# Optimization experiments

Measured on AMD Instinct MI355X. Metric: run time of the kernel, lower is better.

The kernel has to match this reference:

```python
import jax, jax.numpy as jnp
import numpy as np

TEMPERATURE = 0.1

def setup_inputs() -> dict:
    key = jax.random.key(0)
    k1, k2 = jax.random.split(key)
    A = jax.random.normal(k1, (16, 2048, 256), dtype=jnp.float32)
    B = jax.random.normal(k2, (16, 2048, 256), dtype=jnp.float32)
    return {"A": A, "B": B}

def _l2norm(x):
    # F.normalize(p=2, dim=-1): x / max(||x||, eps), eps=1e-12
    n = jnp.sqrt(jnp.sum(x * x, axis=-1, keepdims=True))
    return x / jnp.maximum(n, 1e-12)

def _nce_dir(sim):
    # sim: (B, N, N) logits; labels are the diagonal (row n -> col n)
    # mean over all B*N rows of (logsumexp(row) - row[label])
    lse = jax.nn.logsumexp(sim, axis=-1)            # (B, N)
    diag = jnp.diagonal(sim, axis1=-2, axis2=-1)    # (B, N)
    return jnp.mean(lse - diag)

def reference(A, B):
    emb1 = _l2norm(A)
    emb2 = _l2norm(B)
    sim12 = jnp.einsum("bnc,bmc->bnm", emb1, emb2) / TEMPERATURE  # (B, N, N)
    # sim21 is sim12 transposed per batch; reuse instead of a second bmm
    sim21 = jnp.swapaxes(sim12, -1, -2)
    return _nce_dir(sim12) + _nce_dir(sim21)
```

## Files before the change

### kernel.cpp

```cpp
#include <hip/hip_runtime.h>
#include <hip/hip_bf16.h>

typedef __attribute__((ext_vector_type(8))) __bf16 bf16x8;
typedef __attribute__((ext_vector_type(16))) float f32x16;

#define SCALE_L2E 14.4269504088896f
#define NTOT 32768

#define AS_GLOBAL __attribute__((address_space(1)))
#define AS_LDS    __attribute__((address_space(3)))

__device__ inline void async_copy16(const void* g, void* l) {
    __builtin_amdgcn_global_load_lds((const AS_GLOBAL void*)g, (AS_LDS void*)l, 16, 0, 0);
}

__device__ inline unsigned int f2bf(float f) {
    unsigned int u = __builtin_bit_cast(unsigned int, f);
    u += 0x7fffu + ((u >> 16) & 1u);
    return u >> 16;
}

__device__ inline uint4 pack8(float4 x, float4 y, float s) {
    uint4 r;
    r.x = f2bf(x.x * s) | (f2bf(x.y * s) << 16);
    r.y = f2bf(x.z * s) | (f2bf(x.w * s) << 16);
    r.z = f2bf(y.x * s) | (f2bf(y.y * s) << 16);
    r.w = f2bf(y.z * s) | (f2bf(y.w * s) << 16);
    return r;
}

__device__ inline float sum8(float4 x, float4 y) {
    return x.x + x.y + x.z + x.w + y.x + y.y + y.z + y.w;
}
__device__ inline float dot8(float4 x, float4 y) {
    return x.x*y.x + x.y*y.y + x.z*y.z + x.w*y.w;
}

__global__ __launch_bounds__(256) void nrm_kernel(
        const float* __restrict__ A, const float* __restrict__ B,
        uint4* __restrict__ E1f, uint4* __restrict__ E2f,
        float* __restrict__ diagPart) {
    const int tid = threadIdx.x, w = tid >> 6, l = tid & 63;
    const int q = l & 31, h = l >> 5;
    const int wid = blockIdx.x * 4 + w;

    const float4* A4 = (const float4*)A + ((size_t)wid * 8 + h) * 64 + q * 2;
    const float4* B4 = (const float4*)B + ((size_t)wid * 8 + h) * 64 + q * 2;

    float ddAcc = 0.f;
    float4 a0 = A4[0], a1 = A4[1], b0 = B4[0], b1 = B4[1];

    #pragma unroll
    for (int i = 0; i < 4; ++i) {
        float4 na0, na1, nb0, nb1;
        if (i < 3) {
            const float4* An = A4 + (i + 1) * 128;
            const float4* Bn = B4 + (i + 1) * 128;
            na0 = An[0]; na1 = An[1]; nb0 = Bn[0]; nb1 = Bn[1];
        }
        float sa = dot8(a0, a0) + dot8(a1, a1);
        float sb = dot8(b0, b0) + dot8(b1, b1);
        float dd = dot8(a0, b0) + dot8(a1, b1);
        #pragma unroll
        for (int off = 1; off <= 16; off <<= 1) {
            sa += __shfl_xor(sa, off);
            sb += __shfl_xor(sb, off);
            dd += __shfl_xor(dd, off);
        }
        const float ia = 1.0f / fmaxf(sqrtf(sa), 1e-12f);
        const float ib = 1.0f / fmaxf(sqrtf(sb), 1e-12f);
        if (q == 0) ddAcc += dd * ia * ib * 10.0f;

        const int n0 = wid * 8 + i * 2 + h;
        const size_t chunk = (size_t)(n0 >> 11) * 65536
                           + (size_t)((n0 & 2047) >> 5) * 1024
                           + (q >> 1) * 64 + (q & 1) * 32 + (n0 & 31);
        E1f[chunk] = pack8(a0, a1, ia);
        E2f[chunk] = pack8(b0, b1, ib);

        a0 = na0; a1 = na1; b0 = nb0; b1 = nb1;
    }

    #pragma unroll
    for (int off = 1; off <= 32; off <<= 1) ddAcc += __shfl_xor(ddAcc, off);
    __shared__ float part[4];
    if (l == 0) part[w] = ddAcc;
    __syncthreads();
    if (tid == 0) diagPart[blockIdx.x] = part[0] + part[1] + part[2] + part[3];
}

__global__ __launch_bounds__(256, 2) void gemm_kernel(
        const bf16x8* __restrict__ E1f, const uint4* __restrict__ E2f,
        float* __restrict__ colSum, float* __restrict__ rowSum) {
    __shared__ bf16x8 Bbuf[2][1024];
    __shared__ float colLDS[2048];

    const int tid = threadIdx.x, w = tid >> 6, l = tid & 63;
    const int rt = blockIdx.x, ct = blockIdx.y, b = blockIdx.z;

    for (int i = l; i < 512; i += 64) colLDS[w * 512 + i] = 0.f;

    const bf16x8* Af0 = E1f + (size_t)b * 65536 + (size_t)(rt * 8 + w * 2) * 1024 + l;
    const bf16x8* Af1 = Af0 + 1024;
    bf16x8 af0[16], af1[16];
    #pragma unroll
    for (int kt = 0; kt < 16; ++kt) { af0[kt] = Af0[kt * 64]; af1[kt] = Af1[kt * 64]; }

    float rowAcc0[16], rowAcc1[16];
    #pragma unroll
    for (int r = 0; r < 16; ++r) { rowAcc0[r] = 0.f; rowAcc1[r] = 0.f; }

    const uint4* Bb = E2f + (size_t)b * 65536 + (size_t)ct * 16384 + l;

    auto stage = [&](int buf, int cg) {
        const uint4* src = Bb + (size_t)cg * 1024 + (w * 4) * 64;
        #pragma unroll
        for (int j = 0; j < 4; ++j)
            async_copy16(src + j * 64, &Bbuf[buf][(w * 4 + j) * 64]);
    };

    stage(0, 0);
    __syncthreads();

    for (int cg = 0; cg < 16; ++cg) {
        if (cg < 15) stage((cg + 1) & 1, cg + 1);

        const bf16x8* Bf = Bbuf[cg & 1];
        f32x16 acc0, acc1;
        #pragma unroll
        for (int r = 0; r < 16; ++r) { acc0[r] = 0.f; acc1[r] = 0.f; }

        #pragma unroll
        for (int kt = 0; kt < 16; ++kt) {
            bf16x8 bfrag = Bf[kt * 64 + l];
            acc0 = __builtin_amdgcn_mfma_f32_32x32x16_bf16(af0[kt], bfrag, acc0, 0, 0, 0);
            acc1 = __builtin_amdgcn_mfma_f32_32x32x16_bf16(af1[kt], bfrag, acc1, 0, 0, 0);
        }

        float p = 0.f;
        #pragma unroll
        for (int r = 0; r < 16; ++r) {
            float e0 = exp2f(fmaf(acc0[r], SCALE_L2E, -SCALE_L2E));
            float e1 = exp2f(fmaf(acc1[r], SCALE_L2E, -SCALE_L2E));
            rowAcc0[r] += e0;
            rowAcc1[r] += e1;
            p += e0 + e1;
        }
        p += __shfl_xor(p, 32);
        if (l < 32) colLDS[w * 512 + cg * 32 + l] += p;
        __syncthreads();
    }

    #pragma unroll
    for (int r = 0; r < 16; ++r) {
        #pragma unroll
        for (int off = 1; off <= 16; off <<= 1) {
            rowAcc0[r] += __shfl_xor(rowAcc0[r], off);
            rowAcc1[r] += __shfl_xor(rowAcc1[r], off);
        }
    }
    if ((l & 31) == 0) {
        float* rs = rowSum + (size_t)b * 2048 + rt * 256 + w * 64 + 4 * (l >> 5);
        #pragma unroll
        for (int r = 0; r < 16; ++r) {
            const int rl = (r & 3) + 8 * (r >> 2);
            atomicAdd(&rs[rl], rowAcc0[r]);
            atomicAdd(&rs[rl + 32], rowAcc1[r]);
        }
    }

    float* gcol = colSum + (size_t)b * 2048 + ct * 512;
    for (int i = tid; i < 512; i += 256) {
        float s = colLDS[i] + colLDS[512 + i] + colLDS[1024 + i] + colLDS[1536 + i];
        atomicAdd(&gcol[i], s);
    }
}

__global__ __launch_bounds__(256) void fin1_kernel(
        const float* __restrict__ red, float* __restrict__ scalars) {
    const int tid = threadIdx.x;
    float s = 0.f;
    #pragma unroll
    for (int k = 0; k < 4; ++k)
        s += logf(red[blockIdx.x * 1024 + k * 256 + tid]);
    #pragma unroll
    for (int off = 1; off <= 32; off <<= 1) s += __shfl_xor(s, off);
    __shared__ float part[4];
    if ((tid & 63) == 0) part[tid >> 6] = s;
    __syncthreads();
    if (tid == 0)
        atomicAdd(&scalars[0], part[0] + part[1] + part[2] + part[3]);
}

__global__ __launch_bounds__(256) void fin2_kernel(
        const float* __restrict__ diagPart, const float* __restrict__ scalars,
        float* __restrict__ out) {
    const int tid = threadIdx.x;
    float d = 0.f;
    for (int i = tid; i < 1024; i += 256) d += diagPart[i];
    #pragma unroll
    for (int off = 1; off <= 32; off <<= 1) d += __shfl_xor(d, off);
    __shared__ float part[4];
    if ((tid & 63) == 0) part[tid >> 6] = d;
    __syncthreads();
    if (tid == 0) {
        const float diag = part[0] + part[1] + part[2] + part[3];
        out[0] = (scalars[0] - 2.0f * diag) / (float)NTOT + 20.0f;
    }
}

extern "C" void kernel_launch(void* const* d_in, const int* in_sizes, int n_in,
                              void* d_out, int out_size, void* d_ws, size_t ws_size,
                              hipStream_t stream) {
    const float* A = (const float*)d_in[0];
    const float* B = (const float*)d_in[1];

    char* w = (char*)d_ws;
    uint4* E1f = (uint4*)w;
    uint4* E2f = (uint4*)(w + (size_t)16 * 1024 * 1024);
    float* colSum = (float*)(w + (size_t)32 * 1024 * 1024);
    float* rowSum = colSum + NTOT;
    float* scalars = rowSum + NTOT;
    float* diagPart = scalars + 2;

    hipMemsetAsync(colSum, 0, (size_t)(2 * NTOT + 2) * 4, stream);

    hipLaunchKernelGGL(nrm_kernel, dim3(1024), dim3(256), 0, stream,
                       A, B, E1f, E2f, diagPart);
    hipLaunchKernelGGL(gemm_kernel, dim3(8, 4, 16), dim3(256), 0, stream,
                       (const bf16x8*)E1f, (const uint4*)E2f, colSum, rowSum);
    hipLaunchKernelGGL(fin1_kernel, dim3(64), dim3(256), 0, stream,
                       colSum, scalars);
    hipLaunchKernelGGL(fin2_kernel, dim3(1), dim3(256), 0, stream,
                       diagPart, scalars, (float*)d_out);
}
```

Baseline: 160.4 us.

## Triple-buffer GEMM staging, drop memset and atomics, fuse finalize kernels

The memset is removed. Global atomics on row and column sums are replaced by per-tile partial buffers that a single fused finalize kernel reduces, and the last block, found through a counter, finishes the diagonal term. The GEMM moves to a 3-deep async LDS ring with explicit vmcnt waits and one barrier per step. The nrm kernel issues all loads up front and folds the exp scale into E1, which removes an FMA per element. The grid is flattened so the batch index varies fastest. This cuts launches and atomic contention, at the cost of extra partial-buffer traffic and more LDS.

Result: slower. 291.2 us (+81.5%).

```diff
diff --git a/kernel.cpp b/kernel.cpp
--- a/kernel.cpp
+++ b/kernel.cpp
@@ -29,9 +29,6 @@
     return r;
 }
 
-__device__ inline float sum8(float4 x, float4 y) {
-    return x.x + x.y + x.z + x.w + y.x + y.y + y.z + y.w;
-}
 __device__ inline float dot8(float4 x, float4 y) {
     return x.x*y.x + x.y*y.y + x.z*y.z + x.w*y.w;
 }
@@ -39,7 +36,8 @@
 __global__ __launch_bounds__(256) void nrm_kernel(
         const float* __restrict__ A, const float* __restrict__ B,
         uint4* __restrict__ E1f, uint4* __restrict__ E2f,
-        float* __restrict__ diagPart) {
+        float* __restrict__ diagPart, float* __restrict__ scalars,
+        unsigned int* __restrict__ counter) {
     const int tid = threadIdx.x, w = tid >> 6, l = tid & 63;
     const int q = l & 31, h = l >> 5;
     const int wid = blockIdx.x * 4 + w;
@@ -47,20 +45,21 @@
     const float4* A4 = (const float4*)A + ((size_t)wid * 8 + h) * 64 + q * 2;
     const float4* B4 = (const float4*)B + ((size_t)wid * 8 + h) * 64 + q * 2;
 
+    float4 a[8], bb[8];
+    #pragma unroll
+    for (int i = 0; i < 4; ++i) {
+        a[2*i]    = A4[i * 128];
+        a[2*i+1]  = A4[i * 128 + 1];
+        bb[2*i]   = B4[i * 128];
+        bb[2*i+1] = B4[i * 128 + 1];
+    }
+
     float ddAcc = 0.f;
-    float4 a0 = A4[0], a1 = A4[1], b0 = B4[0], b1 = B4[1];
-
     #pragma unroll
     for (int i = 0; i < 4; ++i) {
-        float4 na0, na1, nb0, nb1;
-        if (i < 3) {
-            const float4* An = A4 + (i + 1) * 128;
-            const float4* Bn = B4 + (i + 1) * 128;
-            na0 = An[0]; na1 = An[1]; nb0 = Bn[0]; nb1 = Bn[1];
-        }
-        float sa = dot8(a0, a0) + dot8(a1, a1);
-        float sb = dot8(b0, b0) + dot8(b1, b1);
-        float dd = dot8(a0, b0) + dot8(a1, b1);
+        float sa = dot8(a[2*i], a[2*i]) + dot8(a[2*i+1], a[2*i+1]);
+        float sb = dot8(bb[2*i], bb[2*i]) + dot8(bb[2*i+1], bb[2*i+1]);
+        float dd = dot8(a[2*i], bb[2*i]) + dot8(a[2*i+1], bb[2*i+1]);
         #pragma unroll
         for (int off = 1; off <= 16; off <<= 1) {
             sa += __shfl_xor(sa, off);
@@ -75,10 +74,8 @@
         const size_t chunk = (size_t)(n0 >> 11) * 65536
                            + (size_t)((n0 & 2047) >> 5) * 1024
                            + (q >> 1) * 64 + (q & 1) * 32 + (n0 & 31);
-        E1f[chunk] = pack8(a0, a1, ia);
-        E2f[chunk] = pack8(b0, b1, ib);
-
-        a0 = na0; a1 = na1; b0 = nb0; b1 = nb1;
+        E1f[chunk] = pack8(a[2*i], a[2*i+1], ia * SCALE_L2E);
+        E2f[chunk] = pack8(bb[2*i], bb[2*i+1], ib);
     }
 
     #pragma unroll
@@ -87,16 +84,18 @@
     if (l == 0) part[w] = ddAcc;
     __syncthreads();
     if (tid == 0) diagPart[blockIdx.x] = part[0] + part[1] + part[2] + part[3];
+    if (blockIdx.x == 0 && tid == 0) { scalars[0] = 0.f; *counter = 0u; }
 }
 
 __global__ __launch_bounds__(256, 2) void gemm_kernel(
         const bf16x8* __restrict__ E1f, const uint4* __restrict__ E2f,
-        float* __restrict__ colSum, float* __restrict__ rowSum) {
-    __shared__ bf16x8 Bbuf[2][1024];
+        float* __restrict__ colPart, float* __restrict__ rowPart) {
+    __shared__ bf16x8 Bbuf[3][1024];
     __shared__ float colLDS[2048];
 
     const int tid = threadIdx.x, w = tid >> 6, l = tid & 63;
-    const int rt = blockIdx.x, ct = blockIdx.y, b = blockIdx.z;
+    const int rt = blockIdx.x >> 6;
+    const int ct = (blockIdx.x >> 4) & 3, b = blockIdx.x & 15;
 
     for (int i = l; i < 512; i += 64) colLDS[w * 512 + i] = 0.f;
 
@@ -120,12 +119,16 @@
     };
 
     stage(0, 0);
-    __syncthreads();
-
+    stage(1, 1);
+
+    #pragma unroll
     for (int cg = 0; cg < 16; ++cg) {
-        if (cg < 15) stage((cg + 1) & 1, cg + 1);
-
-        const bf16x8* Bf = Bbuf[cg & 1];
+        if (cg < 15) asm volatile("s_waitcnt vmcnt(4)" ::: "memory");
+        else         asm volatile("s_waitcnt vmcnt(0)" ::: "memory");
+        __builtin_amdgcn_s_barrier();
+        if (cg < 14) stage((cg + 2) % 3, cg + 2);
+
+        const bf16x8* Bf = Bbuf[cg % 3];
         f32x16 acc0, acc1;
         #pragma unroll
         for (int r = 0; r < 16; ++r) { acc0[r] = 0.f; acc1[r] = 0.f; }
@@ -140,15 +143,14 @@
         float p = 0.f;
         #pragma unroll
         for (int r = 0; r < 16; ++r) {
-            float e0 = exp2f(fmaf(acc0[r], SCALE_L2E, -SCALE_L2E));
-            float e1 = exp2f(fmaf(acc1[r], SCALE_L2E, -SCALE_L2E));
+            float e0 = exp2f(acc0[r] - SCALE_L2E);
+            float e1 = exp2f(acc1[r] - SCALE_L2E);
             rowAcc0[r] += e0;
             rowAcc1[r] += e1;
             p += e0 + e1;
         }
         p += __shfl_xor(p, 32);
         if (l < 32) colLDS[w * 512 + cg * 32 + l] += p;
-        __syncthreads();
     }
 
     #pragma unroll
@@ -160,52 +162,62 @@
         }
     }
     if ((l & 31) == 0) {
-        float* rs = rowSum + (size_t)b * 2048 + rt * 256 + w * 64 + 4 * (l >> 5);
+        float* rs = rowPart + (size_t)(b * 4 + ct) * 2048 + rt * 256 + w * 64 + 4 * (l >> 5);
         #pragma unroll
         for (int r = 0; r < 16; ++r) {
             const int rl = (r & 3) + 8 * (r >> 2);
-            atomicAdd(&rs[rl], rowAcc0[r]);
-            atomicAdd(&rs[rl + 32], rowAcc1[r]);
-        }
-    }
-
-    float* gcol = colSum + (size_t)b * 2048 + ct * 512;
-    for (int i = tid; i < 512; i += 256) {
-        float s = colLDS[i] + colLDS[512 + i] + colLDS[1024 + i] + colLDS[1536 + i];
-        atomicAdd(&gcol[i], s);
-    }
-}
-
-__global__ __launch_bounds__(256) void fin1_kernel(
-        const float* __restrict__ red, float* __restrict__ scalars) {
+            rs[rl]      = rowAcc0[r];
+            rs[rl + 32] = rowAcc1[r];
+        }
+    }
+
+    __syncthreads();
+    float* gcol = colPart + (size_t)((b * 4 + ct) * 8 + rt) * 512;
+    for (int i = tid; i < 512; i += 256)
+        gcol[i] = colLDS[i] + colLDS[512 + i] + colLDS[1024 + i] + colLDS[1536 + i];
+}
+
+__global__ __launch_bounds__(256) void fin_kernel(
+        const float* __restrict__ colPart, const float* __restrict__ rowPart,
+        const float* __restrict__ diagPart, float* __restrict__ scalars,
+        unsigned int* __restrict__ counter, float* __restrict__ out) {
     const int tid = threadIdx.x;
     float s = 0.f;
     #pragma unroll
-    for (int k = 0; k < 4; ++k)
-        s += logf(red[blockIdx.x * 1024 + k * 256 + tid]);
+    for (int k = 0; k < 2; ++k) {
+        const int g = blockIdx.x * 512 + k * 256 + tid;
+        const float* cp = colPart + (size_t)(((g >> 11) * 4 + ((g >> 9) & 3)) * 8) * 512 + (g & 511);
+        float cs = 0.f;
+        #pragma unroll
+        for (int rt = 0; rt < 8; ++rt) cs += cp[rt * 512];
+        const float* rp = rowPart + (size_t)(g >> 11) * 4 * 2048 + (g & 2047);
+        float rsum = rp[0] + rp[2048] + rp[4096] + rp[6144];
+        s += logf(cs) + logf(rsum);
+    }
     #pragma unroll
     for (int off = 1; off <= 32; off <<= 1) s += __shfl_xor(s, off);
     __shared__ float part[4];
+    __shared__ unsigned int lastFlag;
     if ((tid & 63) == 0) part[tid >> 6] = s;
     __syncthreads();
-    if (tid == 0)
+    if (tid == 0) {
         atomicAdd(&scalars[0], part[0] + part[1] + part[2] + part[3]);
-}
-
-__global__ __launch_bounds__(256) void fin2_kernel(
-        const float* __restrict__ diagPart, const float* __restrict__ scalars,
-        float* __restrict__ out) {
-    const int tid = threadIdx.x;
-    float d = 0.f;
-    for (int i = tid; i < 1024; i += 256) d += diagPart[i];
-    #pragma unroll
-    for (int off = 1; off <= 32; off <<= 1) d += __shfl_xor(d, off);
-    __shared__ float part[4];
-    if ((tid & 63) == 0) part[tid >> 6] = d;
-    __syncthreads();
-    if (tid == 0) {
-        const float diag = part[0] + part[1] + part[2] + part[3];
-        out[0] = (scalars[0] - 2.0f * diag) / (float)NTOT + 20.0f;
+        __threadfence();
+        lastFlag = (atomicAdd(counter, 1u) == 63u) ? 1u : 0u;
+    }
+    __syncthreads();
+    if (lastFlag) {
+        float d = diagPart[tid] + diagPart[tid + 256]
+                + diagPart[tid + 512] + diagPart[tid + 768];
+        #pragma unroll
+        for (int off = 1; off <= 32; off <<= 1) d += __shfl_xor(d, off);
+        if ((tid & 63) == 0) part[tid >> 6] = d;
+        __syncthreads();
+        if (tid == 0) {
+            const float diag = part[0] + part[1] + part[2] + part[3];
+            const float logSum = atomicAdd(&scalars[0], 0.f);
+            out[0] = (logSum - 2.0f * diag) / (float)NTOT + 20.0f;
+        }
     }
 }
 
@@ -218,19 +230,16 @@
     char* w = (char*)d_ws;
     uint4* E1f = (uint4*)w;
     uint4* E2f = (uint4*)(w + (size_t)16 * 1024 * 1024);
-    float* colSum = (float*)(w + (size_t)32 * 1024 * 1024);
-    float* rowSum = colSum + NTOT;
-    float* scalars = rowSum + NTOT;
-    float* diagPart = scalars + 2;
-
-    hipMemsetAsync(colSum, 0, (size_t)(2 * NTOT + 2) * 4, stream);
+    float* colPart = (float*)(w + (size_t)32 * 1024 * 1024);
+    float* rowPart = colPart + 262144;
+    float* diagPart = rowPart + 131072;
+    float* scalars = diagPart + 1024;
+    unsigned int* counter = (unsigned int*)(scalars + 1);
 
     hipLaunchKernelGGL(nrm_kernel, dim3(1024), dim3(256), 0, stream,
-                       A, B, E1f, E2f, diagPart);
-    hipLaunchKernelGGL(gemm_kernel, dim3(8, 4, 16), dim3(256), 0, stream,
-                       (const bf16x8*)E1f, (const uint4*)E2f, colSum, rowSum);
-    hipLaunchKernelGGL(fin1_kernel, dim3(64), dim3(256), 0, stream,
-                       colSum, scalars);
-    hipLaunchKernelGGL(fin2_kernel, dim3(1), dim3(256), 0, stream,
-                       diagPart, scalars, (float*)d_out);
-}
+                       A, B, E1f, E2f, diagPart, scalars, counter);
+    hipLaunchKernelGGL(gemm_kernel, dim3(512), dim3(256), 0, stream,
+                       (const bf16x8*)E1f, (const uint4*)E2f, colPart, rowPart);
+    hipLaunchKernelGGL(fin_kernel, dim3(64), dim3(256), 0, stream,
+                       colPart, rowPart, diagPart, scalars, counter, (float*)d_out);
+}
```

## Fold softmax scale into E1, seed accumulators with bias, use native exp/log

Applied to the files above, without the earlier changes.

Folds the temperature times log2(e) scale into the normalized E1 embedding and starts the MFMA accumulators at -scale, which removes the per-element FMA before each exp2. It also switches to native exp2/log intrinsics and stages twice as many B columns per double-buffer step, halving the barriers. Other changes: a flattened grid with batch as the fastest index for a different block order, and nontemporal loads that issue all input loads up front in the normalize kernel. Risks are a bit more rounding from scaling before the bf16 conversion and from the approximate intrinsics, plus more LDS per block, which could affect occupancy.

New measurement: 163.3 us. About the same (+1.8%).

```diff
diff --git a/kernel.cpp b/kernel.cpp
--- a/kernel.cpp
+++ b/kernel.cpp
@@ -3,8 +3,10 @@
 
 typedef __attribute__((ext_vector_type(8))) __bf16 bf16x8;
 typedef __attribute__((ext_vector_type(16))) float f32x16;
+typedef __attribute__((ext_vector_type(4))) float f32x4;
 
 #define SCALE_L2E 14.4269504088896f
+#define LN2 0.6931471805599453f
 #define NTOT 32768
 
 #define AS_GLOBAL __attribute__((address_space(1)))
@@ -12,6 +14,22 @@
 
 __device__ inline void async_copy16(const void* g, void* l) {
     __builtin_amdgcn_global_load_lds((const AS_GLOBAL void*)g, (AS_LDS void*)l, 16, 0, 0);
+}
+
+__device__ inline float fast_exp2(float x) {
+#if __has_builtin(__builtin_amdgcn_exp2f)
+    return __builtin_amdgcn_exp2f(x);
+#else
+    return exp2f(x);
+#endif
+}
+
+__device__ inline float fast_ln(float x) {
+#if __has_builtin(__builtin_amdgcn_logf)
+    return __builtin_amdgcn_logf(x) * LN2;
+#else
+    return logf(x);
+#endif
 }
 
 __device__ inline unsigned int f2bf(float f) {
@@ -20,7 +38,7 @@
     return u >> 16;
 }
 
-__device__ inline uint4 pack8(float4 x, float4 y, float s) {
+__device__ inline uint4 pack8(f32x4 x, f32x4 y, float s) {
     uint4 r;
     r.x = f2bf(x.x * s) | (f2bf(x.y * s) << 16);
     r.y = f2bf(x.z * s) | (f2bf(x.w * s) << 16);
@@ -29,10 +47,7 @@
     return r;
 }
 
-__device__ inline float sum8(float4 x, float4 y) {
-    return x.x + x.y + x.z + x.w + y.x + y.y + y.z + y.w;
-}
-__device__ inline float dot8(float4 x, float4 y) {
+__device__ inline float dot8(f32x4 x, f32x4 y) {
     return x.x*y.x + x.y*y.y + x.z*y.z + x.w*y.w;
 }
 
@@ -44,23 +59,24 @@
     const int q = l & 31, h = l >> 5;
     const int wid = blockIdx.x * 4 + w;
 
-    const float4* A4 = (const float4*)A + ((size_t)wid * 8 + h) * 64 + q * 2;
-    const float4* B4 = (const float4*)B + ((size_t)wid * 8 + h) * 64 + q * 2;
+    const f32x4* A4 = (const f32x4*)A + ((size_t)wid * 8 + h) * 64 + q * 2;
+    const f32x4* B4 = (const f32x4*)B + ((size_t)wid * 8 + h) * 64 + q * 2;
+
+    f32x4 a[8], bb[8];
+    #pragma unroll
+    for (int i = 0; i < 4; ++i) {
+        a[2*i]    = __builtin_nontemporal_load(A4 + i * 128);
+        a[2*i+1]  = __builtin_nontemporal_load(A4 + i * 128 + 1);
+        bb[2*i]   = __builtin_nontemporal_load(B4 + i * 128);
+        bb[2*i+1] = __builtin_nontemporal_load(B4 + i * 128 + 1);
+    }
 
     float ddAcc = 0.f;
-    float4 a0 = A4[0], a1 = A4[1], b0 = B4[0], b1 = B4[1];
-
     #pragma unroll
     for (int i = 0; i < 4; ++i) {
-        float4 na0, na1, nb0, nb1;
-        if (i < 3) {
-            const float4* An = A4 + (i + 1) * 128;
-            const float4* Bn = B4 + (i + 1) * 128;
-            na0 = An[0]; na1 = An[1]; nb0 = Bn[0]; nb1 = Bn[1];
-        }
-        float sa = dot8(a0, a0) + dot8(a1, a1);
-        float sb = dot8(b0, b0) + dot8(b1, b1);
-        float dd = dot8(a0, b0) + dot8(a1, b1);
+        float sa = dot8(a[2*i], a[2*i]) + dot8(a[2*i+1], a[2*i+1]);
+        float sb = dot8(bb[2*i], bb[2*i]) + dot8(bb[2*i+1], bb[2*i+1]);
+        float dd = dot8(a[2*i], bb[2*i]) + dot8(a[2*i+1], bb[2*i+1]);
         #pragma unroll
         for (int off = 1; off <= 16; off <<= 1) {
             sa += __shfl_xor(sa, off);
@@ -75,10 +91,8 @@
         const size_t chunk = (size_t)(n0 >> 11) * 65536
                            + (size_t)((n0 & 2047) >> 5) * 1024
                            + (q >> 1) * 64 + (q & 1) * 32 + (n0 & 31);
-        E1f[chunk] = pack8(a0, a1, ia);
-        E2f[chunk] = pack8(b0, b1, ib);
-
-        a0 = na0; a1 = na1; b0 = nb0; b1 = nb1;
+        E1f[chunk] = pack8(a[2*i], a[2*i+1], ia * SCALE_L2E);
+        E2f[chunk] = pack8(bb[2*i], bb[2*i+1], ib);
     }
 
     #pragma unroll
@@ -92,13 +106,25 @@
 __global__ __launch_bounds__(256, 2) void gemm_kernel(
         const bf16x8* __restrict__ E1f, const uint4* __restrict__ E2f,
         float* __restrict__ colSum, float* __restrict__ rowSum) {
-    __shared__ bf16x8 Bbuf[2][1024];
+    __shared__ bf16x8 Bbuf[2][2048];
     __shared__ float colLDS[2048];
 
     const int tid = threadIdx.x, w = tid >> 6, l = tid & 63;
-    const int rt = blockIdx.x, ct = blockIdx.y, b = blockIdx.z;
+    const int b = blockIdx.x & 15;
+    const int ct = (blockIdx.x >> 4) & 3, rt = blockIdx.x >> 6;
 
     for (int i = l; i < 512; i += 64) colLDS[w * 512 + i] = 0.f;
+
+    const uint4* Bb = E2f + (size_t)b * 65536 + (size_t)ct * 16384 + l;
+
+    auto stage = [&](int buf, int sg) {
+        const uint4* src = Bb + (size_t)sg * 2048 + (w * 8) * 64;
+        #pragma unroll
+        for (int j = 0; j < 8; ++j)
+            async_copy16(src + j * 64, &Bbuf[buf][(w * 8 + j) * 64]);
+    };
+
+    stage(0, 0);
 
     const bf16x8* Af0 = E1f + (size_t)b * 65536 + (size_t)(rt * 8 + w * 2) * 1024 + l;
     const bf16x8* Af1 = Af0 + 1024;
@@ -110,44 +136,38 @@
     #pragma unroll
     for (int r = 0; r < 16; ++r) { rowAcc0[r] = 0.f; rowAcc1[r] = 0.f; }
 
-    const uint4* Bb = E2f + (size_t)b * 65536 + (size_t)ct * 16384 + l;
-
-    auto stage = [&](int buf, int cg) {
-        const uint4* src = Bb + (size_t)cg * 1024 + (w * 4) * 64;
-        #pragma unroll
-        for (int j = 0; j < 4; ++j)
-            async_copy16(src + j * 64, &Bbuf[buf][(w * 4 + j) * 64]);
-    };
-
-    stage(0, 0);
-    __syncthreads();
-
-    for (int cg = 0; cg < 16; ++cg) {
-        if (cg < 15) stage((cg + 1) & 1, cg + 1);
-
-        const bf16x8* Bf = Bbuf[cg & 1];
-        f32x16 acc0, acc1;
-        #pragma unroll
-        for (int r = 0; r < 16; ++r) { acc0[r] = 0.f; acc1[r] = 0.f; }
-
-        #pragma unroll
-        for (int kt = 0; kt < 16; ++kt) {
-            bf16x8 bfrag = Bf[kt * 64 + l];
-            acc0 = __builtin_amdgcn_mfma_f32_32x32x16_bf16(af0[kt], bfrag, acc0, 0, 0, 0);
-            acc1 = __builtin_amdgcn_mfma_f32_32x32x16_bf16(af1[kt], bfrag, acc1, 0, 0, 0);
-        }
-
-        float p = 0.f;
-        #pragma unroll
-        for (int r = 0; r < 16; ++r) {
-            float e0 = exp2f(fmaf(acc0[r], SCALE_L2E, -SCALE_L2E));
-            float e1 = exp2f(fmaf(acc1[r], SCALE_L2E, -SCALE_L2E));
-            rowAcc0[r] += e0;
-            rowAcc1[r] += e1;
-            p += e0 + e1;
-        }
-        p += __shfl_xor(p, 32);
-        if (l < 32) colLDS[w * 512 + cg * 32 + l] += p;
+    __syncthreads();
+
+    for (int sg = 0; sg < 8; ++sg) {
+        if (sg < 7) stage((sg + 1) & 1, sg + 1);
+
+        const bf16x8* Bf = Bbuf[sg & 1];
+        for (int half = 0; half < 2; ++half) {
+            f32x16 acc0, acc1;
+            #pragma unroll
+            for (int r = 0; r < 16; ++r) {
+                acc0[r] = -SCALE_L2E; acc1[r] = -SCALE_L2E;
+            }
+
+            #pragma unroll
+            for (int kt = 0; kt < 16; ++kt) {
+                bf16x8 bfrag = Bf[half * 1024 + kt * 64 + l];
+                acc0 = __builtin_amdgcn_mfma_f32_32x32x16_bf16(af0[kt], bfrag, acc0, 0, 0, 0);
+                acc1 = __builtin_amdgcn_mfma_f32_32x32x16_bf16(af1[kt], bfrag, acc1, 0, 0, 0);
+            }
+
+            float p = 0.f;
+            #pragma unroll
+            for (int r = 0; r < 16; ++r) {
+                float e0 = fast_exp2(acc0[r]);
+                float e1 = fast_exp2(acc1[r]);
+                rowAcc0[r] += e0;
+                rowAcc1[r] += e1;
+                p += e0 + e1;
+            }
+            p += __shfl_xor(p, 32);
+            if (l < 32) colLDS[w * 512 + (sg * 2 + half) * 32 + l] += p;
+        }
         __syncthreads();
     }
 
@@ -169,6 +189,7 @@
         }
     }
 
+    __syncthreads();
     float* gcol = colSum + (size_t)b * 2048 + ct * 512;
     for (int i = tid; i < 512; i += 256) {
         float s = colLDS[i] + colLDS[512 + i] + colLDS[1024 + i] + colLDS[1536 + i];
@@ -182,7 +203,7 @@
     float s = 0.f;
     #pragma unroll
     for (int k = 0; k < 4; ++k)
-        s += logf(red[blockIdx.x * 1024 + k * 256 + tid]);
+        s += fast_ln(red[blockIdx.x * 1024 + k * 256 + tid]);
     #pragma unroll
     for (int off = 1; off <= 32; off <<= 1) s += __shfl_xor(s, off);
     __shared__ float part[4];
@@ -227,7 +248,7 @@
 
     hipLaunchKernelGGL(nrm_kernel, dim3(1024), dim3(256), 0, stream,
                        A, B, E1f, E2f, diagPart);
-    hipLaunchKernelGGL(gemm_kernel, dim3(8, 4, 16), dim3(256), 0, stream,
+    hipLaunchKernelGGL(gemm_kernel, dim3(512), dim3(256), 0, stream,
                        (const bf16x8*)E1f, (const uint4*)E2f, colSum, rowSum);
     hipLaunchKernelGGL(fin1_kernel, dim3(64), dim3(256), 0, stream,
                        colSum, scalars);
```
